# Optimization experiments

Hardware: AMD Instinct MI355X
Metric: run time of the kernel (lower is better)

## Reference

```python
import jax, jax.numpy as jnp
import numpy as np

B, V, T, F, H = 32, 16, 64, 64, 512
NBINS = 36  # 360 / delta (delta_cog = delta_rb = 10)
OUT = 4     # output_size


def setup_inputs() -> dict:
    key = jax.random.key(0)
    ks = jax.random.split(key, 12)
    s = 1.0 / np.sqrt(H)
    return {
        'sequence': jax.random.normal(ks[0], (B, V, T, F), jnp.float32),
        'dist_matrix': jax.random.uniform(ks[1], (B, V, T, V), jnp.float32),
        'rb_matrix': jax.random.randint(ks[2], (B, V, T, V), 0, NBINS).astype(jnp.int32),
        'cog_matrix': jax.random.randint(ks[3], (B, V, T, V), 0, NBINS).astype(jnp.int32),
        'seq_mask': jnp.ones((B, V, T), jnp.float32),
        'maxval': jax.random.uniform(ks[4], (B, F), jnp.float32) + 1.0,
        'minval': jax.random.uniform(ks[5], (B, F), jnp.float32),
        # per-vessel LSTMCell params (PyTorch gate order i,f,g,o stacked along 4H)
        'W_ih': jax.random.normal(ks[6], (V, 4 * H, F), jnp.float32) * s,
        'W_hh': jax.random.normal(ks[7], (V, 4 * H, H), jnp.float32) * s,
        'b_ih': jnp.zeros((V, 4 * H), jnp.float32),
        'b_hh': jnp.zeros((V, 4 * H), jnp.float32),
        # hardwired attention domain table [360/delta_cog, 360/delta_rb]
        'domain': jax.random.normal(ks[8], (NBINS, NBINS), jnp.float32),
        # per-vessel softAttention linear (2H -> H)
        'soft_W': jax.random.normal(ks[9], (V, H, 2 * H), jnp.float32) * s,
        'soft_b': jnp.zeros((V, H), jnp.float32),
        # shared output linear (H -> F)
        'out_W': jax.random.normal(ks[10], (F, H), jnp.float32) * s,
        'out_b': jnp.zeros((F,), jnp.float32),
    }


def _forward(sequence, dist_matrix, rb_matrix, cog_matrix, seq_mask, maxval, minval,
             W_ih, W_hh, b_ih, b_hh, domain, soft_W, soft_b, out_W, out_b):
    B_, V_, T_, F_ = sequence.shape
    H_ = W_hh.shape[-1]

    def hardwired(h, r, d, m, cg):
        # h: [B,V,H]; r,d,cg: [B,V,V]; m: [B,V]
        mul1 = m[:, :, None] * m[:, None, :]
        mul2 = domain[cg, r]
        w = jax.nn.relu(mul2 - d) * mul1
        w = w / jax.lax.stop_gradient(jnp.max(w))  # torch: weights /= weights.data.max()
        return jnp.einsum('bvw,bwh->bvh', w, h)

    def lstm_step(x, h, c):
        # vectorized over V independent LSTMCells
        g = (jnp.einsum('bvf,vgf->bvg', x, W_ih)
             + jnp.einsum('bvh,vgh->bvg', h, W_hh) + b_ih + b_hh)
        i, f, gg, o = jnp.split(g, 4, axis=-1)
        c_new = jax.nn.sigmoid(f) * c + jax.nn.sigmoid(i) * jnp.tanh(gg)
        h_new = jax.nn.sigmoid(o) * jnp.tanh(c_new)
        return h_new, c_new

    h0 = jnp.zeros((B_, V_, H_), sequence.dtype)
    c0 = jnp.zeros((B_, V_, H_), sequence.dtype)
    xs = (jnp.moveaxis(sequence, 2, 0), jnp.moveaxis(rb_matrix, 2, 0),
          jnp.moveaxis(dist_matrix, 2, 0), jnp.moveaxis(seq_mask, 2, 0),
          jnp.moveaxis(cog_matrix, 2, 0))

    def enc_step(carry, xt):
        h, c = carry
        x, r, d, m, cg = xt
        wh = hardwired(h, r, d, m, cg)
        h, c = lstm_step(x, wh, c)
        return (h, c), h

    (h, c), enc = jax.lax.scan(enc_step, (h0, c0), xs)
    enc = jnp.moveaxis(enc, 0, 2)  # encodedInput [B,V,T,H]

    # decoder, prediction step i=0 (prediction_length=1)
    wh = hardwired(h, rb_matrix[:, :, -1], dist_matrix[:, :, -1],
                   seq_mask[:, :, -1], cog_matrix[:, :, -1])
    # get_previous_sequence: denormalize under no_grad
    prev = jax.lax.stop_gradient(
        sequence[:, :, -1] * (maxval - minval)[:, None, :] + minval[:, None, :])
    h, c = lstm_step(prev, wh, c)

    # per-vessel softAttention
    score = jnp.einsum('bvth,bvh->bvt', enc, h)
    alpha = jax.nn.softmax(score * seq_mask, axis=-1)
    ctx = jnp.einsum('bvt,bvth->bvh', alpha, enc)
    # faithful to torch.stack((ctx, h)).view(B, 2H) memory-reinterpret per vessel
    z = jnp.moveaxis(jnp.stack([ctx, h], axis=0), 2, 0).reshape(V_, B_, 2 * H_)
    h = jnp.moveaxis(
        jnp.tanh(jnp.einsum('vbk,vhk->vbh', z, soft_W) + soft_b[:, None, :]), 0, 1)

    out = jax.nn.relu(jnp.einsum('bvh,fh->bvf', h, out_W) + out_b)
    return out[:, :, None, :OUT]  # [B, V, prediction_length=1, output_size]


def reference(sequence, dist_matrix, rb_matrix, cog_matrix, seq_mask, maxval, minval,
              W_ih, W_hh, b_ih, b_hh, domain, soft_W, soft_b, out_W, out_b,
              maxVessels=V):
    return _forward(sequence, dist_matrix, rb_matrix, cog_matrix, seq_mask,
                    maxval, minval, W_ih, W_hh, b_ih, b_hh, domain,
                    soft_W, soft_b, out_W, out_b)
```

## Files before the change

kernel.cpp:

```cpp
#include <hip/hip_runtime.h>
#include <math.h>

#define B 32
#define V 16
#define T 64
#define F 64
#define H 512
#define NB 36
#define G4H 2048

typedef unsigned short u16;
typedef unsigned long long ull;
typedef __attribute__((ext_vector_type(8))) short bf16x8;
typedef __attribute__((ext_vector_type(4))) float f32x4;

#define OFF_H0     0
#define OFF_H1     262144
#define OFF_C      524288
#define OFF_CNT    786432
#define OFF_WALL   819200
#define OFF_CTX    819200
#define OFF_HSOFT  1081344
#define OFF_WMAX   1343488
#define OFF_WHSTG  1343552
#define OFF_SEQSTG 1605696
#define OFF_WSTG   2670656
#define OFF_ENC    12107840

#define WHP 262144
#define WLDS_BYTES 147456
#define HFLAG_BASE 16384

__device__ __forceinline__ float sigmoidf_(float x) { return 1.0f / (1.0f + __expf(-x)); }

__device__ __forceinline__ u16 f2bf(float f) {
    union { float f; unsigned u; } x; x.f = f;
    unsigned r = x.u + 0x7FFF + ((x.u >> 16) & 1);
    return (u16)(r >> 16);
}
__device__ __forceinline__ float bf2f(u16 u) {
    union { unsigned i; float f; } x; x.i = ((unsigned)u) << 16;
    return x.f;
}
__device__ __forceinline__ f32x4 mfma16(bf16x8 a, bf16x8 b, f32x4 c) {
    return __builtin_amdgcn_mfma_f32_16x16x32_bf16(a, b, c, 0, 0, 0);
}
__device__ __forceinline__ bf16x8 mk_bf16x8(ull lo, ull hi) {
    union { ull u[2]; bf16x8 v; } x; x.u[0] = lo; x.u[1] = hi; return x.v;
}
__device__ __forceinline__ bf16x8 mk_bf16x8q(uint4 q) {
    union { uint4 q; bf16x8 v; } x; x.q = q; return x.v;
}

__device__ __forceinline__ ull ld_agent(const ull* p) {
    return __hip_atomic_load((ull*)p, __ATOMIC_RELAXED, __HIP_MEMORY_SCOPE_AGENT);
}
__device__ __forceinline__ void st_agent(ull* p, ull x) {
    __hip_atomic_store(p, x, __ATOMIC_RELAXED, __HIP_MEMORY_SCOPE_AGENT);
}
__device__ __forceinline__ void st_agent_f(float* p, float x) {
    __hip_atomic_store(p, x, __ATOMIC_RELAXED, __HIP_MEMORY_SCOPE_AGENT);
}
__device__ __forceinline__ void st_agent_u32(unsigned* p, unsigned x) {
    __hip_atomic_store(p, x, __ATOMIC_RELAXED, __HIP_MEMORY_SCOPE_AGENT);
}
__device__ __forceinline__ unsigned ld_agent_u32(const unsigned* p) {
    return __hip_atomic_load((unsigned*)p, __ATOMIC_RELAXED, __HIP_MEMORY_SCOPE_AGENT);
}

#define NZB 3200
#define NHW 64
#define NWC 4608
#define NSS 1040
__global__ __launch_bounds__(256) void k_prep(
    float* __restrict__ ws,
    const float* __restrict__ dist, const int* __restrict__ rb,
    const int* __restrict__ cog, const float* __restrict__ mask,
    const float* __restrict__ domain, float* __restrict__ w_all,
    float* __restrict__ wmax_all,
    const float* __restrict__ W_ih, const float* __restrict__ W_hh,
    u16* __restrict__ Wstg,
    const float* __restrict__ seq, const float* __restrict__ maxval,
    const float* __restrict__ minval, u16* __restrict__ seqstg) {
    __shared__ float red[256];
    int bid = blockIdx.x;
    int tid = threadIdx.x;

    if (bid < NZB) {
        ws[bid * 256 + tid] = 0.0f;
        return;
    }
    if (bid < NZB + NHW) {
        int t = bid - NZB;
        float lmax = 0.0f;
        for (int idx = tid; idx < B * V * V; idx += 256) {
            int b = idx >> 8;
            int rem = idx & 255;
            int i = rem >> 4, j = rem & 15;
            int base = ((b * V + i) * T + t) * V + j;
            float val = domain[cog[base] * NB + rb[base]] - dist[base];
            val = val > 0.0f ? val : 0.0f;
            val *= mask[(b * V + i) * T + t] * mask[(b * V + j) * T + t];
            w_all[t * (B * V * V) + idx] = val;
            lmax = fmaxf(lmax, val);
        }
        red[tid] = lmax;
        __syncthreads();
        for (int s = 128; s > 0; s >>= 1) {
            if (tid < s) red[tid] = fmaxf(red[tid], red[tid + s]);
            __syncthreads();
        }
        if (tid == 0) wmax_all[t] = red[0];
        return;
    }
    if (bid < NZB + NHW + NWC) {
        int idx = bid - (NZB + NHW);
        int v = idx / 288, hk = (idx / 18) & 15, ks = idx % 18;
#pragma unroll
        for (int s = 0; s < 2; ++s) {
            int slot = tid + s * 256;
            int nt = slot >> 6, lane = slot & 63;
            int g = nt >> 1, hh = nt & 1;
            int col = g * H + hk * 32 + hh * 16 + (lane & 15);
            int k = ks * 32 + ((lane >> 4) << 3);
            const float* src = (k < F) ? &W_ih[(v * G4H + col) * F + k]
                                       : &W_hh[(v * G4H + col) * H + (k - F)];
            float4 x0 = *(const float4*)src;
            float4 x1 = *(const float4*)(src + 4);
            union { u16 u[8]; uint4 q; } pk;
            pk.u[0] = f2bf(x0.x); pk.u[1] = f2bf(x0.y); pk.u[2] = f2bf(x0.z); pk.u[3] = f2bf(x0.w);
            pk.u[4] = f2bf(x1.x); pk.u[5] = f2bf(x1.y); pk.u[6] = f2bf(x1.z); pk.u[7] = f2bf(x1.w);
            *(uint4*)&Wstg[(size_t)((((v * 16 + hk) * 18 + ks) * 8 + nt) * 64 + lane) * 8] = pk.q;
        }
        return;
    }
    {
        int idx = bid - (NZB + NHW + NWC);
        int v = idx / 65, t = idx % 65;
        int mt = tid >> 7, ks = (tid >> 6) & 1, lane = tid & 63;
        int b = mt * 16 + (lane & 15);
        int f = ks * 32 + ((lane >> 4) << 3);
        union { u16 u[8]; uint4 q; } pk;
        if (t < T) {
            const float* sp = &seq[((b * V + v) * T + t) * F + f];
            float4 x0 = *(const float4*)sp, x1 = *(const float4*)(sp + 4);
            pk.u[0] = f2bf(x0.x); pk.u[1] = f2bf(x0.y); pk.u[2] = f2bf(x0.z); pk.u[3] = f2bf(x0.w);
            pk.u[4] = f2bf(x1.x); pk.u[5] = f2bf(x1.y); pk.u[6] = f2bf(x1.z); pk.u[7] = f2bf(x1.w);
        } else {
            const float* sp = &seq[((b * V + v) * T + (T - 1)) * F + f];
            float4 x0 = *(const float4*)sp, x1 = *(const float4*)(sp + 4);
            float4 mx0 = *(const float4*)&maxval[b * F + f], mx1 = *(const float4*)&maxval[b * F + f + 4];
            float4 mn0 = *(const float4*)&minval[b * F + f], mn1 = *(const float4*)&minval[b * F + f + 4];
            pk.u[0] = f2bf(x0.x * (mx0.x - mn0.x) + mn0.x);
            pk.u[1] = f2bf(x0.y * (mx0.y - mn0.y) + mn0.y);
            pk.u[2] = f2bf(x0.z * (mx0.z - mn0.z) + mn0.z);
            pk.u[3] = f2bf(x0.w * (mx0.w - mn0.w) + mn0.w);
            pk.u[4] = f2bf(x1.x * (mx1.x - mn1.x) + mn1.x);
            pk.u[5] = f2bf(x1.y * (mx1.y - mn1.y) + mn1.y);
            pk.u[6] = f2bf(x1.z * (mx1.z - mn1.z) + mn1.z);
            pk.u[7] = f2bf(x1.w * (mx1.w - mn1.w) + mn1.w);
        }
        *(uint4*)&seqstg[(((size_t)(t * 16 + v)) * 4 + mt * 2 + ks) * 512 + lane * 8] = pk.q;
    }
}

__global__ __launch_bounds__(256) void k_recur(
    const u16* __restrict__ seqstg, const u16* __restrict__ Wstg,
    const float* __restrict__ w_all, const float* __restrict__ wmax_all,
    const float* __restrict__ b_ih, const float* __restrict__ b_hh,
    float* __restrict__ h0buf, float* __restrict__ h1buf,
    float* __restrict__ c, u16* __restrict__ enc, u16* __restrict__ whstg,
    unsigned* __restrict__ bar) {
    extern __shared__ u16 Wlds[];

    int bid = blockIdx.x;
    int v = bid & 15, hk = bid >> 4;
    int tid = threadIdx.x;

    {
        const uint4* wsrc = (const uint4*)(Wstg + (size_t)((v * 16 + hk) * 18) * 4096);
        uint4* wdst = (uint4*)Wlds;
        for (int i = tid; i < 9216; i += 256) wdst[i] = wsrc[i];
    }

    int lane = tid & 63, w = tid >> 6;
    int mtw = w & 1, hh = w >> 1;
    int col = hk * 32 + hh * 16 + (lane & 15);
    int q4 = (lane >> 4) << 2;
    float bi = b_ih[v * G4H + col] + b_hh[v * G4H + col];
    float bf_ = b_ih[v * G4H + H + col] + b_hh[v * G4H + H + col];
    float bg_ = b_ih[v * G4H + 2 * H + col] + b_hh[v * G4H + 2 * H + col];
    float bo = b_ih[v * G4H + 3 * H + col] + b_hh[v * G4H + 3 * H + col];

    unsigned* a_sig = bar + (bid * 4 + w) * 16;
    unsigned* h_sig = bar + HFLAG_BASE + (bid * 4 + w) * 16;
    unsigned* h_poll = bar + HFLAG_BASE +
        (((hk * 16 + (lane >> 1)) * 4) + ((w >> 1) + (lane & 1) * 2)) * 16;
    unsigned* a_poll = bar +
        ((((lane >> 1) * 16 + v) * 4) + (2 * mtw + (lane & 1))) * 16;

    int a_b = tid >> 3;
    int a_cq = tid & 7;
    const int wh_idx = ((((v * 2 + (a_b >> 4)) * 16 + hk) * 64 +
                         (((a_cq >> 1) << 4) + (a_b & 15))) * 8 + (a_cq & 1) * 4);

    __syncthreads();

    for (int t = 0; t <= T; ++t) {
        int par = t & 1;
        int tm = t < T ? t : (T - 1);
        const float* hin = (t & 1) ? h0buf : h1buf;
        float* hout = (t & 1) ? h1buf : h0buf;

        uint4 s0 = *(const uint4*)&seqstg[(((size_t)(t * 16 + v)) * 4 + mtw * 2 + 0) * 512 + lane * 8];
        uint4 s1 = *(const uint4*)&seqstg[(((size_t)(t * 16 + v)) * 4 + mtw * 2 + 1) * 512 + lane * 8];
        float inv = 1.0f / wmax_all[tm];
        const float* wrow = &w_all[(size_t)tm * (B * V * V) + (a_b * V + v) * V];
        float4 wr0 = *(const float4*)(wrow);
        float4 wr1 = *(const float4*)(wrow + 4);
        float4 wr2 = *(const float4*)(wrow + 8);
        float4 wr3 = *(const float4*)(wrow + 12);
        float cprev[4];
#pragma unroll
        for (int r = 0; r < 4; ++r)
            cprev[r] = c[((mtw * 16 + q4 + r) * V + v) * H + col];

        f32x4 acc[4];
        acc[0][0] = bi;  acc[0][1] = bi;  acc[0][2] = bi;  acc[0][3] = bi;
        acc[1][0] = bf_; acc[1][1] = bf_; acc[1][2] = bf_; acc[1][3] = bf_;
        acc[2][0] = bg_; acc[2][1] = bg_; acc[2][2] = bg_; acc[2][3] = bg_;
        acc[3][0] = bo;  acc[3][1] = bo;  acc[3][2] = bo;  acc[3][3] = bo;
        {
            bf16x8 a0f = mk_bf16x8q(s0);
            bf16x8 a1f = mk_bf16x8q(s1);
#pragma unroll
            for (int g = 0; g < 4; ++g)
                acc[g] = mfma16(a0f, *(const bf16x8*)&Wlds[(0 * 8 + (g * 2 + hh)) * 512 + lane * 8], acc[g]);
#pragma unroll
            for (int g = 0; g < 4; ++g)
                acc[g] = mfma16(a1f, *(const bf16x8*)&Wlds[(1 * 8 + (g * 2 + hh)) * 512 + lane * 8], acc[g]);
        }

        if (t > 0) {
            if (lane < 32) {
                while (ld_agent_u32(h_poll) < (unsigned)t) {}
            }
            __builtin_amdgcn_sched_barrier(0);
        }

        {
            const ull* hb = (const ull*)&hin[(a_b * V) * H + hk * 32 + a_cq * 4];
            float a0 = 0.f, a1 = 0.f, a2 = 0.f, a3 = 0.f;
            const float wj[16] = {wr0.x, wr0.y, wr0.z, wr0.w, wr1.x, wr1.y, wr1.z, wr1.w,
                                  wr2.x, wr2.y, wr2.z, wr2.w, wr3.x, wr3.y, wr3.z, wr3.w};
#pragma unroll
            for (int j = 0; j < 16; ++j) {
                ull lo = ld_agent(hb + (size_t)j * (H / 2));
                ull hi = ld_agent(hb + (size_t)j * (H / 2) + 1);
                union { ull u; float f[2]; } u0, u1;
                u0.u = lo; u1.u = hi;
                a0 = fmaf(wj[j], u0.f[0], a0);
                a1 = fmaf(wj[j], u0.f[1], a1);
                a2 = fmaf(wj[j], u1.f[0], a2);
                a3 = fmaf(wj[j], u1.f[1], a3);
            }
            union { u16 u[4]; ull q; } pk;
            pk.u[0] = f2bf(a0 * inv); pk.u[1] = f2bf(a1 * inv);
            pk.u[2] = f2bf(a2 * inv); pk.u[3] = f2bf(a3 * inv);
            st_agent((ull*)&whstg[par * WHP + wh_idx], pk.q);
        }
        __builtin_amdgcn_s_waitcnt(0);
        __builtin_amdgcn_sched_barrier(0);
        if (lane == 0) st_agent_u32(a_sig, (unsigned)(t + 1));

        if (lane < 32) {
            while (ld_agent_u32(a_poll) < (unsigned)(t + 1)) {}
        }
        __builtin_amdgcn_sched_barrier(0);

        bf16x8 afr[16];
#pragma unroll
        for (int ksw = 0; ksw < 16; ++ksw) {
            const ull* src = (const ull*)&whstg[par * WHP + (((v * 2 + mtw) * 16 + ksw) * 64 + lane) * 8];
            ull lo = ld_agent(src), hi = ld_agent(src + 1);
            afr[ksw] = mk_bf16x8(lo, hi);
        }
#pragma unroll
        for (int ks = 0; ks < 16; ++ks) {
#pragma unroll
            for (int g = 0; g < 4; ++g) {
                bf16x8 wfr = *(const bf16x8*)&Wlds[((ks + 2) * 8 + (g * 2 + hh)) * 512 + lane * 8];
                acc[g] = mfma16(afr[ks], wfr, acc[g]);
            }
        }

        float cnv[4], hnv[4];
#pragma unroll
        for (int r = 0; r < 4; ++r) {
            float gi = acc[0][r];
            float gf = acc[1][r];
            float gg = acc[2][r];
            float go = acc[3][r];
            cnv[r] = sigmoidf_(gf) * cprev[r] + sigmoidf_(gi) * tanhf(gg);
            hnv[r] = sigmoidf_(go) * tanhf(cnv[r]);
            int b = mtw * 16 + q4 + r;
            st_agent_f(&hout[(b * V + v) * H + col], hnv[r]);
        }
        if (t < T) {
            __builtin_amdgcn_s_waitcnt(0);
            __builtin_amdgcn_sched_barrier(0);
            if (lane == 0) st_agent_u32(h_sig, (unsigned)(t + 1));
        }

#pragma unroll
        for (int r = 0; r < 4; ++r) {
            int b = mtw * 16 + q4 + r;
            c[(b * V + v) * H + col] = cnv[r];
            if (t < T) enc[((size_t)(b * V + v) * T + t) * H + col] = f2bf(hnv[r]);
        }
    }
}

__global__ __launch_bounds__(256) void k_attn(
    const u16* __restrict__ enc, const float* __restrict__ h,
    const float* __restrict__ mask, float* __restrict__ ctx) {
    int bid = blockIdx.x;
    int b = bid >> 4, v = bid & 15;
    int tid = threadIdx.x;
    int wave = tid >> 6, lane = tid & 63;
    __shared__ float hs[H];
    __shared__ float sc[T];
    __shared__ float al[T];
    const u16* encbase = enc + (size_t)((b * V + v) * T) * H;
    const float* hb = h + (b * V + v) * H;
    for (int i = tid; i < H; i += 256) hs[i] = hb[i];
    __syncthreads();
    for (int tt = wave; tt < T; tt += 4) {
        const u16* e = encbase + tt * H;
        float p = 0.0f;
#pragma unroll
        for (int ii = 0; ii < 8; ++ii) p += bf2f(e[ii * 64 + lane]) * hs[ii * 64 + lane];
        for (int off = 32; off; off >>= 1) p += __shfl_down(p, off, 64);
        if (lane == 0) sc[tt] = p;
    }
    __syncthreads();
    if (tid < 64) {
        float m_t = mask[(b * V + v) * T + tid];
        float s = sc[tid] * m_t;
        float mx = s;
        for (int off = 32; off; off >>= 1) mx = fmaxf(mx, __shfl_xor(mx, off, 64));
        float e = __expf(s - mx);
        float sum = e;
        for (int off = 32; off; off >>= 1) sum += __shfl_xor(sum, off, 64);
        al[tid] = e / sum;
    }
    __syncthreads();
    for (int hh = tid; hh < H; hh += 256) {
        float a = 0.0f;
        for (int tt = 0; tt < T; ++tt) a += al[tt] * bf2f(encbase[tt * H + hh]);
        ctx[(b * V + v) * H + hh] = a;
    }
}

__global__ __launch_bounds__(256) void k_soft(
    const float* __restrict__ ctx, const float* __restrict__ hdec,
    const float* __restrict__ soft_W, const float* __restrict__ soft_b,
    float* __restrict__ hsoft) {
    int v = blockIdx.x;
    int h0 = blockIdx.y * 32;
    int tid = threadIdx.x;
    int cg = tid & 31, rg = tid >> 5;
    __shared__ float sA[32][36];
    __shared__ float sW2[32][36];
    float* sAf = &sA[0][0];
    float* sWf = &sW2[0][0];
    float acc[4] = {0.f, 0.f, 0.f, 0.f};
    int arow = tid >> 3, akq = tid & 7;
    float4 areg, wreg;

    {
        int k = akq * 4;
        const float* src = (arow < 16) ? ctx : hdec;
        int bsrc = 2 * (arow & 15) + (k >= H ? 1 : 0);
        areg = *(const float4*)&src[(bsrc * V + v) * H + (k & (H - 1))];
        wreg = *(const float4*)&soft_W[(v * H + h0 + arow) * (2 * H) + k];
    }
    for (int kc = 0; kc < 2 * H; kc += 32) {
        __syncthreads();
        *(float4*)&sAf[arow * 36 + akq * 4] = areg;
        *(float4*)&sWf[arow * 36 + akq * 4] = wreg;
        __syncthreads();
        if (kc + 32 < 2 * H) {
            int k = kc + 32 + akq * 4;
            const float* src = (arow < 16) ? ctx : hdec;
            int bsrc = 2 * (arow & 15) + (k >= H ? 1 : 0);
            areg = *(const float4*)&src[(bsrc * V + v) * H + (k & (H - 1))];
            wreg = *(const float4*)&soft_W[(v * H + h0 + arow) * (2 * H) + kc + 32 + akq * 4];
        }
#pragma unroll
        for (int k4 = 0; k4 < 8; ++k4) {
            float4 wv = *(const float4*)&sWf[cg * 36 + k4 * 4];
            float4 a0 = *(const float4*)&sAf[(rg * 4 + 0) * 36 + k4 * 4];
            float4 a1 = *(const float4*)&sAf[(rg * 4 + 1) * 36 + k4 * 4];
            float4 a2 = *(const float4*)&sAf[(rg * 4 + 2) * 36 + k4 * 4];
            float4 a3 = *(const float4*)&sAf[(rg * 4 + 3) * 36 + k4 * 4];
            acc[0] += a0.x * wv.x + a0.y * wv.y + a0.z * wv.z + a0.w * wv.w;
            acc[1] += a1.x * wv.x + a1.y * wv.y + a1.z * wv.z + a1.w * wv.w;
            acc[2] += a2.x * wv.x + a2.y * wv.y + a2.z * wv.z + a2.w * wv.w;
            acc[3] += a3.x * wv.x + a3.y * wv.y + a3.z * wv.z + a3.w * wv.w;
        }
    }
    float bb = soft_b[v * H + h0 + cg];
#pragma unroll
    for (int r = 0; r < 4; ++r) {
        int row = rg * 4 + r;
        hsoft[(row * V + v) * H + h0 + cg] = tanhf(acc[r] + bb);
    }
}

__global__ __launch_bounds__(64) void k_out(
    const float* __restrict__ hsoft, const float* __restrict__ outW,
    const float* __restrict__ outb, float* __restrict__ out) {
    int bid = blockIdx.x;
    int b = bid >> 4, v = bid & 15;
    int lane = threadIdx.x;
    const float* hb = hsoft + (b * V + v) * H;
    float p[4] = {0.0f, 0.0f, 0.0f, 0.0f};
#pragma unroll
    for (int ii = 0; ii < 8; ++ii) {
        float hv = hb[ii * 64 + lane];
#pragma unroll
        for (int o = 0; o < 4; ++o) p[o] += hv * outW[o * H + ii * 64 + lane];
    }
#pragma unroll
    for (int o = 0; o < 4; ++o) {
        float s = p[o];
        for (int off = 32; off; off >>= 1) s += __shfl_down(s, off, 64);
        if (lane == 0) {
            float val = s + outb[o];
            out[(b * V + v) * 4 + o] = val > 0.0f ? val : 0.0f;
        }
    }
}

extern "C" void kernel_launch(void* const* d_in, const int* in_sizes, int n_in,
                              void* d_out, int out_size, void* d_ws, size_t ws_size,
                              hipStream_t stream) {
    const float* seq = (const float*)d_in[0];
    const float* dist = (const float*)d_in[1];
    const int* rb = (const int*)d_in[2];
    const int* cog = (const int*)d_in[3];
    const float* mask = (const float*)d_in[4];
    const float* maxval = (const float*)d_in[5];
    const float* minval = (const float*)d_in[6];
    const float* W_ih = (const float*)d_in[7];
    const float* W_hh = (const float*)d_in[8];
    const float* b_ih = (const float*)d_in[9];
    const float* b_hh = (const float*)d_in[10];
    const float* domain = (const float*)d_in[11];
    const float* soft_W = (const float*)d_in[12];
    const float* soft_b = (const float*)d_in[13];
    const float* out_W = (const float*)d_in[14];
    const float* out_b = (const float*)d_in[15];

    float* ws = (float*)d_ws;
    float* h0buf = ws + OFF_H0;
    float* h1buf = ws + OFF_H1;
    float* c = ws + OFF_C;
    unsigned* bar = (unsigned*)(ws + OFF_CNT);
    float* w_all = ws + OFF_WALL;
    float* ctx = ws + OFF_CTX;
    float* hsoft = ws + OFF_HSOFT;
    float* wmax_all = ws + OFF_WMAX;
    u16* whstg = (u16*)(ws + OFF_WHSTG);
    u16* seqstg = (u16*)(ws + OFF_SEQSTG);
    u16* Wstg = (u16*)(ws + OFF_WSTG);
    u16* enc = (u16*)(ws + OFF_ENC);

    (void)hipFuncSetAttribute((const void*)k_recur,
                              hipFuncAttributeMaxDynamicSharedMemorySize, WLDS_BYTES);

    k_prep<<<NZB + NHW + NWC + NSS, 256, 0, stream>>>(
        ws, dist, rb, cog, mask, domain, w_all, wmax_all,
        W_ih, W_hh, Wstg, seq, maxval, minval, seqstg);

    k_recur<<<256, 256, WLDS_BYTES, stream>>>(seqstg, Wstg, w_all, wmax_all,
                                              b_ih, b_hh, h0buf, h1buf, c, enc,
                                              whstg, bar);

    k_attn<<<B * V, 256, 0, stream>>>(enc, h0buf, mask, ctx);
    k_soft<<<dim3(16, 16), 256, 0, stream>>>(ctx, h0buf, soft_W, soft_b, hsoft);
    k_out<<<B * V, 64, 0, stream>>>(hsoft, out_W, out_b, (float*)d_out);
}
```

Baseline: 809.5 us.

## Replace per-wave flag signalling with per-block flags and __syncthreads

Per-wave signal and poll flags are replaced by one flag per block. Each block now waits on a __syncthreads, has thread 0 publish its step counter, has 16 threads poll the 16 peer flags with s_sleep, and waits on another __syncthreads. This cuts the number of flag writes and polled cache lines per step and reduces spin pressure on memory. In exchange, every step gains block-wide barriers, and wave-level overlap is lost because a block waits for its slowest wave. Correctness also relies on __syncthreads ordering the agent-scope stores before the flag store, which replaces the explicit waitcnt.

```diff
diff --git a/kernel.cpp b/kernel.cpp
--- a/kernel.cpp
+++ b/kernel.cpp
@@ -29,7 +29,6 @@
 
 #define WHP 262144
 #define WLDS_BYTES 147456
-#define HFLAG_BASE 16384
 
 __device__ __forceinline__ float sigmoidf_(float x) { return 1.0f / (1.0f + __expf(-x)); }
 
@@ -183,8 +182,8 @@
         for (int i = tid; i < 9216; i += 256) wdst[i] = wsrc[i];
     }
 
-    int lane = tid & 63, w = tid >> 6;
-    int mtw = w & 1, hh = w >> 1;
+    int lane = tid & 63, wvi = tid >> 6;
+    int mtw = wvi & 1, hh = wvi >> 1;
     int col = hk * 32 + hh * 16 + (lane & 15);
     int q4 = (lane >> 4) << 2;
     float bi = b_ih[v * G4H + col] + b_hh[v * G4H + col];
@@ -192,12 +191,10 @@
     float bg_ = b_ih[v * G4H + 2 * H + col] + b_hh[v * G4H + 2 * H + col];
     float bo = b_ih[v * G4H + 3 * H + col] + b_hh[v * G4H + 3 * H + col];
 
-    unsigned* a_sig = bar + (bid * 4 + w) * 16;
-    unsigned* h_sig = bar + HFLAG_BASE + (bid * 4 + w) * 16;
-    unsigned* h_poll = bar + HFLAG_BASE +
-        (((hk * 16 + (lane >> 1)) * 4) + ((w >> 1) + (lane & 1) * 2)) * 16;
-    unsigned* a_poll = bar +
-        ((((lane >> 1) * 16 + v) * 4) + (2 * mtw + (lane & 1))) * 16;
+    unsigned* aslot = bar + (v * 16 + hk) * 16;
+    unsigned* bslot = bar + (256 + hk * 16 + v) * 16;
+    unsigned* apoll = bar + (v * 16 + (tid & 15)) * 16;
+    unsigned* bpoll = bar + (256 + hk * 16 + (tid & 15)) * 16;
 
     int a_b = tid >> 3;
     int a_cq = tid & 7;
@@ -242,10 +239,10 @@
         }
 
         if (t > 0) {
-            if (lane < 32) {
-                while (ld_agent_u32(h_poll) < (unsigned)t) {}
+            if (tid < 16) {
+                while (ld_agent_u32(bpoll) < (unsigned)t) __builtin_amdgcn_s_sleep(1);
             }
-            __builtin_amdgcn_sched_barrier(0);
+            __syncthreads();
         }
 
         {
@@ -269,14 +266,13 @@
             pk.u[2] = f2bf(a2 * inv); pk.u[3] = f2bf(a3 * inv);
             st_agent((ull*)&whstg[par * WHP + wh_idx], pk.q);
         }
-        __builtin_amdgcn_s_waitcnt(0);
-        __builtin_amdgcn_sched_barrier(0);
-        if (lane == 0) st_agent_u32(a_sig, (unsigned)(t + 1));
-
-        if (lane < 32) {
-            while (ld_agent_u32(a_poll) < (unsigned)(t + 1)) {}
-        }
-        __builtin_amdgcn_sched_barrier(0);
+        __syncthreads();
+        if (tid == 0) st_agent_u32(aslot, (unsigned)(t + 1));
+
+        if (tid < 16) {
+            while (ld_agent_u32(apoll) < (unsigned)(t + 1)) __builtin_amdgcn_s_sleep(1);
+        }
+        __syncthreads();
 
         bf16x8 afr[16];
 #pragma unroll
@@ -307,9 +303,8 @@
             st_agent_f(&hout[(b * V + v) * H + col], hnv[r]);
         }
         if (t < T) {
-            __builtin_amdgcn_s_waitcnt(0);
-            __builtin_amdgcn_sched_barrier(0);
-            if (lane == 0) st_agent_u32(h_sig, (unsigned)(t + 1));
+            __syncthreads();
+            if (tid == 0) st_agent_u32(bslot, (unsigned)(t + 1));
         }
 
 #pragma unroll
```

New measurement: 700.8 us. 13.4% less time.
